# Optimization experiments

Measured on AMD Instinct MI355X. Metric: run time of the kernel, lower is better.

The kernel has to match this reference:

```python
import jax, jax.numpy as jnp
import numpy as np

N = 2048      # nodes: 8 sequences x 256 tokens
E = 524288    # edges: dense attention graph, 8 * 256^2
H = 8         # heads
DK = 64       # per-head dim


def setup_inputs() -> dict:
    key = jax.random.key(0)
    k1, k2, k3, k4, k5 = jax.random.split(key, 5)
    q = jax.random.normal(k1, (N, H, DK), dtype=jnp.float32)
    k = jax.random.normal(k2, (N, H, DK), dtype=jnp.float32)
    v = jax.random.normal(k3, (N, H, DK), dtype=jnp.float32)
    edge_src = jax.random.randint(k4, (E,), 0, N, dtype=jnp.int32)
    edge_dst = jax.random.randint(k5, (E,), 0, N, dtype=jnp.int32)
    return {"q": q, "k": k, "v": v, "edge_src": edge_src, "edge_dst": edge_dst}


def reference(q, k, v, edge_src, edge_dst):
    # src_dot_dst('k','q','score'): per-edge dot product over head dim -> [E, H]
    score = jnp.einsum('ehd,ehd->eh', k[edge_src], q[edge_dst])
    # scaled_exp('score', sqrt(d_k)): exp(clamp(score / sqrt(d_k), -10, 10))
    score = jnp.exp(jnp.clip(score / jnp.sqrt(jnp.float32(DK)), -10.0, 10.0))
    # send_and_recv: wv = sum_dst(v_src * score), z = sum_dst(score)
    wv = jax.ops.segment_sum(v[edge_src] * score[:, :, None], edge_dst, num_segments=N)  # [N, H, DK]
    z = jax.ops.segment_sum(score, edge_dst, num_segments=N)  # [N, H]
    # post_func normalization: attention output per node
    return wv / z[:, :, None]
```

## Files before the change

kernel.cpp:

```cpp
#include <hip/hip_runtime.h>

#define NNODES 2048
#define NHEAD 8
#define DKDIM 64

typedef unsigned int uint;
typedef unsigned short ushort;
typedef unsigned char uchar;
typedef __fp16 h2 __attribute__((ext_vector_type(2)));
typedef __fp16 h8 __attribute__((ext_vector_type(8)));
typedef float f16v __attribute__((ext_vector_type(16)));

#define KSCALE 0.18033688011112042f
#define CLAMP2 14.426950408889634f

__device__ __forceinline__ uint pk2(float a, float b) {
    union { h2 h; uint u; } x; x.h = __builtin_amdgcn_cvt_pkrtz(a, b); return x.u;
}

__global__ void prep1(const float* __restrict__ k, uint4* __restrict__ kc,
                      uint4* __restrict__ A4) {
    int i = blockIdx.x * 256 + threadIdx.x;
    int dim8 = i & 7, node = (i >> 3) & 2047, h = i >> 14;
    const float* src = k + (size_t)node * 512 + h * 64 + dim8 * 8;
    float4 f0 = *(const float4*)src;
    float4 f1 = *(const float4*)(src + 4);
    uint4 o;
    o.x = pk2(f0.x * KSCALE, f0.y * KSCALE);
    o.y = pk2(f0.z * KSCALE, f0.w * KSCALE);
    o.z = pk2(f1.x * KSCALE, f1.y * KSCALE);
    o.w = pk2(f1.z * KSCALE, f1.w * KSCALE);
    kc[(h * 2048 + node) * 8 + dim8] = o;
    uint4 zz = {0u, 0u, 0u, 0u};
    A4[i] = zz;
    A4[i + 131072] = zz;
}

__global__ void prep2(const float* __restrict__ v, ushort* __restrict__ vt,
                      const int* __restrict__ es, const int* __restrict__ ed,
                      uint* __restrict__ A32, int E) {
    __shared__ float tile[64][65];
    int b = blockIdx.x;
    int t = threadIdx.x;
    if (b < 256) {
        int h = b & 7, tn = b >> 3;
        int nl = t >> 2, dq = (t & 3) * 16;
        const float* src = v + ((size_t)(tn * 64 + nl)) * 512 + h * 64 + dq;
#pragma unroll
        for (int i = 0; i < 4; ++i) {
            float4 f = *(const float4*)(src + i * 4);
            tile[nl][dq + i * 4 + 0] = f.x;
            tile[nl][dq + i * 4 + 1] = f.y;
            tile[nl][dq + i * 4 + 2] = f.z;
            tile[nl][dq + i * 4 + 3] = f.w;
        }
        __syncthreads();
        int dim = t >> 2, nq = (t & 3) * 16;
        uint wv[8];
#pragma unroll
        for (int i = 0; i < 8; ++i)
            wv[i] = pk2(tile[nq + 2 * i][dim], tile[nq + 2 * i + 1][dim]);
        char* base = (char*)vt + ((size_t)(b & 7) * 64 + dim) * 4096 + (b >> 3) * 128;
        int nb0 = (t & 3) * 2;
        uint4 lo = { wv[0], wv[1], wv[2], wv[3] };
        uint4 hi = { wv[4], wv[5], wv[6], wv[7] };
        *(uint4*)(base + nb0 * 16) = lo;
        *(uint4*)(base + nb0 * 16 + 16) = hi;
    } else {
        int i = (b - 256) * 256 + t;
        if (i < E) {
            uint idx = (uint)ed[i] * 2048u + (uint)es[i];
            atomicAdd(&A32[idx >> 2], 1u << ((idx & 3) * 8));
        }
    }
}

__global__ void __launch_bounds__(512, 1) attn_kernel(
    const float* __restrict__ q, const ushort* __restrict__ kc, const ushort* __restrict__ vt,
    const uchar* __restrict__ A8, float* __restrict__ out) {
    __shared__ __align__(16) char LK[2][2][8192];
    __shared__ __align__(16) char LV[2][2][8192];
    __shared__ __align__(16) char LA[2][2][5120];

    int b = blockIdx.x;
    int h = b & 7;
    int dst0 = (b >> 3) * 64;
    int t = threadIdx.x;
    int w = t >> 6, half = w >> 2;
    int u = w & 3, sr = u >> 1, dc = u & 1;
    int l = t & 63, lm = l & 31, hi = l >> 5;
    int ht = t & 255;

    const char* kH = (const char*)kc + (size_t)h * 262144;
    const char* vH = (const char*)vt + (size_t)h * 262144;

    h8 qf[4];
    {
        const float* qp = q + (size_t)(dst0 + dc * 32 + lm) * 512 + h * 64 + hi * 8;
#pragma unroll
        for (int j = 0; j < 4; ++j) {
            float4 f0 = *(const float4*)(qp + j * 16);
            float4 f1 = *(const float4*)(qp + j * 16 + 4);
            union { uint u4[4]; h8 v; } U;
            U.u4[0] = pk2(f0.x, f0.y); U.u4[1] = pk2(f0.z, f0.w);
            U.u4[2] = pk2(f1.x, f1.y); U.u4[3] = pk2(f1.z, f1.w);
            qf[j] = U.v;
        }
    }

    f16v of[2];
#pragma unroll
    for (int dg = 0; dg < 2; ++dg)
#pragma unroll
        for (int i = 0; i < 16; ++i) of[dg][i] = 0.f;
    float z = 0.f;

    int r0 = ht >> 3, b0 = ht & 7;
    int ar_ = ht >> 2, as_ = ht & 3;
    int ts0 = half * 16;
    uint4 kr[2], vr[2], ar;

#pragma unroll
    for (int j = 0; j < 2; ++j) {
        int row = r0 + j * 32;
        kr[j] = *(const uint4*)(kH + (size_t)(ts0 * 64 + row) * 128 + b0 * 16);
        vr[j] = *(const uint4*)(vH + (size_t)row * 4096 + ts0 * 128 + b0 * 16);
        *(uint4*)(LK[half][0] + row * 128 + (b0 ^ (row & 7)) * 16) = kr[j];
        *(uint4*)(LV[half][0] + row * 128 + (b0 ^ (row & 7)) * 16) = vr[j];
    }
    ar = *(const uint4*)(A8 + (size_t)(dst0 + ar_) * 2048 + ts0 * 64 + as_ * 16);
    *(uint4*)(LA[half][0] + ar_ * 80 + as_ * 16) = ar;
    __syncthreads();

    for (int it = 0; it < 16; ++it) {
        int cur = it & 1;
        int ts = ts0 + it;
        if (it < 15) {
#pragma unroll
            for (int j = 0; j < 2; ++j) {
                int row = r0 + j * 32;
                kr[j] = *(const uint4*)(kH + (size_t)((ts + 1) * 64 + row) * 128 + b0 * 16);
                vr[j] = *(const uint4*)(vH + (size_t)row * 4096 + (ts + 1) * 128 + b0 * 16);
            }
            ar = *(const uint4*)(A8 + (size_t)(dst0 + ar_) * 2048 + (ts + 1) * 64 + as_ * 16);
        }

        f16v sacc;
#pragma unroll
        for (int i = 0; i < 16; ++i) sacc[i] = 0.f;
        __builtin_amdgcn_s_setprio(1);
#pragma unroll
        for (int j = 0; j < 4; ++j) {
            h8 kf = *(const h8*)(LK[half][cur] + (sr * 32 + lm) * 128 +
                                 (((2 * j + hi) ^ (lm & 7)) * 16));
            sacc = __builtin_amdgcn_mfma_f32_32x32x16_f16(kf, qf[j], sacc, 0, 0, 0);
        }
        __builtin_amdgcn_s_setprio(0);

        uint W[4][2];
        {
            const char* Ac = LA[half][cur];
#pragma unroll
            for (int G = 0; G < 4; ++G) {
                uint aw = *(const uint*)(Ac + (dc * 32 + lm) * 80 + sr * 32 + G * 8 + 4 * hi);
                float ee[4];
#pragma unroll
                for (int j2 = 0; j2 < 4; ++j2) {
                    float sc = fminf(fmaxf(sacc[4 * G + j2], -CLAMP2), CLAMP2);
                    ee[j2] = exp2f(sc) * (float)((aw >> (8 * j2)) & 255u);
                    z += ee[j2];
                }
                W[G][0] = pk2(ee[0], ee[1]);
                W[G][1] = pk2(ee[2], ee[3]);
            }
        }
        uint Wx[4][2];
#pragma unroll
        for (int G = 0; G < 4; ++G) {
            Wx[G][0] = __shfl_xor(W[G][0], 32);
            Wx[G][1] = __shfl_xor(W[G][1], 32);
        }

        __builtin_amdgcn_s_setprio(1);
#pragma unroll
        for (int ks = 0; ks < 2; ++ks) {
            union { uint u4[4]; h8 v; } S;
            S.u4[0] = hi ? Wx[2 * ks + 1][0] : W[2 * ks][0];
            S.u4[1] = hi ? Wx[2 * ks + 1][1] : W[2 * ks][1];
            S.u4[2] = hi ? W[2 * ks + 1][0] : Wx[2 * ks][0];
            S.u4[3] = hi ? W[2 * ks + 1][1] : Wx[2 * ks][1];
#pragma unroll
            for (int dg = 0; dg < 2; ++dg) {
                h8 vf = *(const h8*)(LV[half][cur] + (dg * 32 + lm) * 128 +
                                     (((sr * 4 + ks * 2 + hi) ^ (lm & 7)) * 16));
                of[dg] = __builtin_amdgcn_mfma_f32_32x32x16_f16(vf, S.v, of[dg], 0, 0, 0);
            }
        }
        __builtin_amdgcn_s_setprio(0);

        if (it < 15) {
            int nb = cur ^ 1;
#pragma unroll
            for (int j = 0; j < 2; ++j) {
                int row = r0 + j * 32;
                *(uint4*)(LK[half][nb] + row * 128 + (b0 ^ (row & 7)) * 16) = kr[j];
                *(uint4*)(LV[half][nb] + row * 128 + (b0 ^ (row & 7)) * 16) = vr[j];
            }
            *(uint4*)(LA[half][nb] + ar_ * 80 + as_ * 16) = ar;
        }
        __syncthreads();
    }

    z += __shfl_xor(z, 32);

    float* CL = (float*)&LK[0][0][0];
    float* CLz = (float*)&LV[0][0][0];
    int gid = half * 2 + sr;
    for (int p = 0; p < 4; ++p) {
        if (gid == p) {
#pragma unroll
            for (int dg = 0; dg < 2; ++dg)
#pragma unroll
                for (int reg = 0; reg < 16; ++reg) {
                    int dim = dg * 32 + (reg & 3) + 8 * (reg >> 2) + 4 * hi;
                    int idx = (dc * 32 + lm) * 68 + dim;
                    if (p == 0) CL[idx] = of[dg][reg];
                    else CL[idx] += of[dg][reg];
                }
            if (hi == 0) {
                if (p == 0) CLz[dc * 32 + lm] = z;
                else CLz[dc * 32 + lm] += z;
            }
        }
        __syncthreads();
    }

    {
        int dst = t >> 3, d8 = t & 7;
        float inv = 1.0f / CLz[dst];
        float4 o0 = *(float4*)(CL + dst * 68 + d8 * 8);
        float4 o1 = *(float4*)(CL + dst * 68 + d8 * 8 + 4);
        o0.x *= inv; o0.y *= inv; o0.z *= inv; o0.w *= inv;
        o1.x *= inv; o1.y *= inv; o1.z *= inv; o1.w *= inv;
        float* op = out + (size_t)(dst0 + dst) * 512 + h * 64 + d8 * 8;
        *(float4*)op = o0;
        *(float4*)(op + 4) = o1;
    }
}


extern "C" void kernel_launch(void* const* d_in, const int* in_sizes, int n_in,
                              void* d_out, int out_size, void* d_ws, size_t ws_size,
                              hipStream_t stream) {
    const float* q = (const float*)d_in[0];
    const float* k = (const float*)d_in[1];
    const float* v = (const float*)d_in[2];
    const int* esrc = (const int*)d_in[3];
    const int* edst = (const int*)d_in[4];
    float* out = (float*)d_out;
    const int E = in_sizes[3];

    uchar* A8 = (uchar*)d_ws;
    ushort* kc = (ushort*)(A8 + (size_t)NNODES * NNODES);
    ushort* vt = kc + (size_t)NHEAD * NNODES * DKDIM;

    prep1<<<512, 256, 0, stream>>>(k, (uint4*)kc, (uint4*)A8);
    prep2<<<2304, 256, 0, stream>>>(v, vt, esrc, edst, (uint*)A8, E);
    attn_kernel<<<256, 512, 0, stream>>>(q, kc, vt, A8, out);
}
```

Baseline: 63.58 us.

## Pack edge-count adjacency matrix into 4-bit nibbles and remap blocks for locality

Measured after the change: 65.30 us. 2.7% more time.

```diff
diff --git a/kernel.cpp b/kernel.cpp
--- a/kernel.cpp
+++ b/kernel.cpp
@@ -33,7 +33,6 @@
     kc[(h * 2048 + node) * 8 + dim8] = o;
     uint4 zz = {0u, 0u, 0u, 0u};
     A4[i] = zz;
-    A4[i + 131072] = zz;
 }
 
 __global__ void prep2(const float* __restrict__ v, ushort* __restrict__ vt,
@@ -70,7 +69,7 @@
         int i = (b - 256) * 256 + t;
         if (i < E) {
             uint idx = (uint)ed[i] * 2048u + (uint)es[i];
-            atomicAdd(&A32[idx >> 2], 1u << ((idx & 3) * 8));
+            atomicAdd(&A32[idx >> 3], 1u << ((idx & 7) * 4));
         }
     }
 }
@@ -83,8 +82,10 @@
     __shared__ __align__(16) char LA[2][2][5120];
 
     int b = blockIdx.x;
-    int h = b & 7;
-    int dst0 = (b >> 3) * 64;
+    int j = b & 7, idx = b >> 3;
+    int dt = (j & 3) * 8 + (idx >> 2);
+    int h = (j >> 2) * 4 + (idx & 3);
+    int dst0 = dt * 64;
     int t = threadIdx.x;
     int w = t >> 6, half = w >> 2;
     int u = w & 3, sr = u >> 1, dc = u & 1;
@@ -98,13 +99,13 @@
     {
         const float* qp = q + (size_t)(dst0 + dc * 32 + lm) * 512 + h * 64 + hi * 8;
 #pragma unroll
-        for (int j = 0; j < 4; ++j) {
-            float4 f0 = *(const float4*)(qp + j * 16);
-            float4 f1 = *(const float4*)(qp + j * 16 + 4);
+        for (int jq = 0; jq < 4; ++jq) {
+            float4 f0 = *(const float4*)(qp + jq * 16);
+            float4 f1 = *(const float4*)(qp + jq * 16 + 4);
             union { uint u4[4]; h8 v; } U;
             U.u4[0] = pk2(f0.x, f0.y); U.u4[1] = pk2(f0.z, f0.w);
             U.u4[2] = pk2(f1.x, f1.y); U.u4[3] = pk2(f1.z, f1.w);
-            qf[j] = U.v;
+            qf[jq] = U.v;
         }
     }
 
@@ -116,20 +117,22 @@
     float z = 0.f;
 
     int r0 = ht >> 3, b0 = ht & 7;
-    int ar_ = ht >> 2, as_ = ht & 3;
+    int arow = ht >> 1, aseg = ht & 1;
     int ts0 = half * 16;
     uint4 kr[2], vr[2], ar;
 
 #pragma unroll
-    for (int j = 0; j < 2; ++j) {
-        int row = r0 + j * 32;
-        kr[j] = *(const uint4*)(kH + (size_t)(ts0 * 64 + row) * 128 + b0 * 16);
-        vr[j] = *(const uint4*)(vH + (size_t)row * 4096 + ts0 * 128 + b0 * 16);
-        *(uint4*)(LK[half][0] + row * 128 + (b0 ^ (row & 7)) * 16) = kr[j];
-        *(uint4*)(LV[half][0] + row * 128 + (b0 ^ (row & 7)) * 16) = vr[j];
-    }
-    ar = *(const uint4*)(A8 + (size_t)(dst0 + ar_) * 2048 + ts0 * 64 + as_ * 16);
-    *(uint4*)(LA[half][0] + ar_ * 80 + as_ * 16) = ar;
+    for (int jj = 0; jj < 2; ++jj) {
+        int row = r0 + jj * 32;
+        kr[jj] = *(const uint4*)(kH + (size_t)(ts0 * 64 + row) * 128 + b0 * 16);
+        vr[jj] = *(const uint4*)(vH + (size_t)row * 4096 + ts0 * 128 + b0 * 16);
+        *(uint4*)(LK[half][0] + row * 128 + (b0 ^ (row & 7)) * 16) = kr[jj];
+        *(uint4*)(LV[half][0] + row * 128 + (b0 ^ (row & 7)) * 16) = vr[jj];
+    }
+    if (ht < 128) {
+        ar = *(const uint4*)(A8 + (size_t)(dst0 + arow) * 1024 + ts0 * 32 + aseg * 16);
+        *(uint4*)(LA[half][0] + arow * 80 + aseg * 16) = ar;
+    }
     __syncthreads();
 
     for (int it = 0; it < 16; ++it) {
@@ -137,12 +140,13 @@
         int ts = ts0 + it;
         if (it < 15) {
 #pragma unroll
-            for (int j = 0; j < 2; ++j) {
-                int row = r0 + j * 32;
-                kr[j] = *(const uint4*)(kH + (size_t)((ts + 1) * 64 + row) * 128 + b0 * 16);
-                vr[j] = *(const uint4*)(vH + (size_t)row * 4096 + (ts + 1) * 128 + b0 * 16);
-            }
-            ar = *(const uint4*)(A8 + (size_t)(dst0 + ar_) * 2048 + (ts + 1) * 64 + as_ * 16);
+            for (int jj = 0; jj < 2; ++jj) {
+                int row = r0 + jj * 32;
+                kr[jj] = *(const uint4*)(kH + (size_t)((ts + 1) * 64 + row) * 128 + b0 * 16);
+                vr[jj] = *(const uint4*)(vH + (size_t)row * 4096 + (ts + 1) * 128 + b0 * 16);
+            }
+            if (ht < 128)
+                ar = *(const uint4*)(A8 + (size_t)(dst0 + arow) * 1024 + (ts + 1) * 32 + aseg * 16);
         }
 
         f16v sacc;
@@ -150,10 +154,10 @@
         for (int i = 0; i < 16; ++i) sacc[i] = 0.f;
         __builtin_amdgcn_s_setprio(1);
 #pragma unroll
-        for (int j = 0; j < 4; ++j) {
+        for (int jq = 0; jq < 4; ++jq) {
             h8 kf = *(const h8*)(LK[half][cur] + (sr * 32 + lm) * 128 +
-                                 (((2 * j + hi) ^ (lm & 7)) * 16));
-            sacc = __builtin_amdgcn_mfma_f32_32x32x16_f16(kf, qf[j], sacc, 0, 0, 0);
+                                 (((2 * jq + hi) ^ (lm & 7)) * 16));
+            sacc = __builtin_amdgcn_mfma_f32_32x32x16_f16(kf, qf[jq], sacc, 0, 0, 0);
         }
         __builtin_amdgcn_s_setprio(0);
 
@@ -162,12 +166,12 @@
             const char* Ac = LA[half][cur];
 #pragma unroll
             for (int G = 0; G < 4; ++G) {
-                uint aw = *(const uint*)(Ac + (dc * 32 + lm) * 80 + sr * 32 + G * 8 + 4 * hi);
+                uint aw = *(const uint*)(Ac + (dc * 32 + lm) * 80 + sr * 16 + G * 4);
                 float ee[4];
 #pragma unroll
                 for (int j2 = 0; j2 < 4; ++j2) {
                     float sc = fminf(fmaxf(sacc[4 * G + j2], -CLAMP2), CLAMP2);
-                    ee[j2] = exp2f(sc) * (float)((aw >> (8 * j2)) & 255u);
+                    ee[j2] = exp2f(sc) * (float)((aw >> (16 * hi + 4 * j2)) & 15u);
                     z += ee[j2];
                 }
                 W[G][0] = pk2(ee[0], ee[1]);
@@ -201,12 +205,13 @@
         if (it < 15) {
             int nb = cur ^ 1;
 #pragma unroll
-            for (int j = 0; j < 2; ++j) {
-                int row = r0 + j * 32;
-                *(uint4*)(LK[half][nb] + row * 128 + (b0 ^ (row & 7)) * 16) = kr[j];
-                *(uint4*)(LV[half][nb] + row * 128 + (b0 ^ (row & 7)) * 16) = vr[j];
-            }
-            *(uint4*)(LA[half][nb] + ar_ * 80 + as_ * 16) = ar;
+            for (int jj = 0; jj < 2; ++jj) {
+                int row = r0 + jj * 32;
+                *(uint4*)(LK[half][nb] + row * 128 + (b0 ^ (row & 7)) * 16) = kr[jj];
+                *(uint4*)(LV[half][nb] + row * 128 + (b0 ^ (row & 7)) * 16) = vr[jj];
+            }
+            if (ht < 128)
+                *(uint4*)(LA[half][nb] + arow * 80 + aseg * 16) = ar;
         }
         __syncthreads();
     }
@@ -223,9 +228,9 @@
 #pragma unroll
                 for (int reg = 0; reg < 16; ++reg) {
                     int dim = dg * 32 + (reg & 3) + 8 * (reg >> 2) + 4 * hi;
-                    int idx = (dc * 32 + lm) * 68 + dim;
-                    if (p == 0) CL[idx] = of[dg][reg];
-                    else CL[idx] += of[dg][reg];
+                    int idx2 = (dc * 32 + lm) * 68 + dim;
+                    if (p == 0) CL[idx2] = of[dg][reg];
+                    else CL[idx2] += of[dg][reg];
                 }
             if (hi == 0) {
                 if (p == 0) CLz[dc * 32 + lm] = z;
@@ -261,7 +266,7 @@
     const int E = in_sizes[3];
 
     uchar* A8 = (uchar*)d_ws;
-    ushort* kc = (ushort*)(A8 + (size_t)NNODES * NNODES);
+    ushort* kc = (ushort*)(A8 + (size_t)NNODES * NNODES / 2);
     ushort* vt = kc + (size_t)NHEAD * NNODES * DKDIM;
 
     prep1<<<512, 256, 0, stream>>>(k, (uint4*)kc, (uint4*)A8);
```
